# Optimization experiments

Hardware: AMD Instinct MI355X
Metric: run time of the kernel (lower is better)

The kernel has to match this reference:

```python
import jax, jax.numpy as jnp
import numpy as np

B, M, C = 8, 8192, 256   # batch, seeds, seed feature dim
F = 128                  # vote feature dim
P, K = 256, 32           # proposals, samples per group
CA, NCLS = 256, 10       # aggregated feat dim, classes
RADIUS = 0.3


def _lin(x, w, b):
    # 1x1 conv == pointwise linear; w: (out, in)
    return jnp.einsum('...c,oc->...o', x, w) + b


def _bnrelu(x, s, t):
    # eval-mode BatchNorm folded to per-channel affine, then ReLU
    return jnp.maximum(x * s + t, 0.0)


def _fps(xyz, npoint):
    # farthest point sampling; deterministic start at index 0
    Bb, N, _ = xyz.shape
    bidx = jnp.arange(Bb)

    def step(carry, _):
        distance, farthest = carry
        centroid = xyz[bidx, farthest][:, None, :]          # (B,1,2)
        d = jnp.sum((xyz - centroid) ** 2, -1)              # (B,N)
        distance = jnp.minimum(distance, d)
        return (distance, jnp.argmax(distance, -1)), farthest

    init = (jnp.full((Bb, N), 1e10, xyz.dtype), jnp.zeros((Bb,), jnp.int32))
    _, idx = jax.lax.scan(step, init, None, length=npoint)
    return jnp.transpose(idx)                               # (B, npoint)


def _ball_query(xyz, new_xyz, radius, nsample):
    # squared-distance cdist (monotone in euclid dist, so same sort order)
    N = xyz.shape[1]
    d2 = (jnp.sum(new_xyz ** 2, -1)[:, :, None]
          + jnp.sum(xyz ** 2, -1)[:, None, :]
          - 2.0 * jnp.einsum('bsd,bnd->bsn', new_xyz, xyz))  # (B,S,N)
    gidx = jnp.broadcast_to(jnp.arange(N), d2.shape)
    # out-of-radius points replaced by group_first (= index 0, as in source)
    gidx = jnp.where(d2 > radius * radius, 0, gidx)
    order = jnp.argsort(d2, axis=-1)
    return jnp.take_along_axis(gidx, order, axis=-1)[:, :, :nsample]


def _gather(points, idx):
    # points: (B,N,C); idx: (B,...) -> (B,...,C)
    return jax.vmap(lambda p, i: p[i])(points, idx)


def _forward(seed_xyz, seed_feats,
             v_off_w1, v_off_b1, v_off_s1, v_off_t1, v_off_w2, v_off_b2,
             v_ft_w1, v_ft_b1, v_ft_s1, v_ft_t1, v_ft_w2, v_ft_b2,
             a_w1, a_b1, a_s1, a_t1, a_w2, a_b2, a_s2, a_t2,
             p_w1, p_b1, p_s1, p_t1, p_w2, p_b2, p_s2, p_t2,
             obj_w, obj_b, cls_w, cls_b):
    # --- VotingModule (vote_factor=1) ---
    h = _bnrelu(_lin(seed_feats, v_off_w1, v_off_b1), v_off_s1, v_off_t1)
    offsets = _lin(h, v_off_w2, v_off_b2)                   # (B,M,2)
    g = _bnrelu(_lin(seed_feats, v_ft_w1, v_ft_b1), v_ft_s1, v_ft_t1)
    vote_feats = _lin(g, v_ft_w2, v_ft_b2)                  # (B,M,F)
    votes_xyz = seed_xyz + offsets                          # (B,M,2)

    # --- VoteAggregation ---
    fps_idx = _fps(votes_xyz, P)                            # (B,P)
    new_xyz = _gather(votes_xyz, fps_idx)                   # (B,P,2)
    gidx = _ball_query(votes_xyz, new_xyz, RADIUS, K)       # (B,P,K)
    gv = _gather(votes_xyz, gidx)                           # (B,P,K,2)
    gf = _gather(vote_feats, gidx)                          # (B,P,K,F)
    comb = jnp.concatenate([gv - new_xyz[:, :, None, :], gf], -1)  # (B,P,K,F+2)
    x = _bnrelu(_lin(comb, a_w1, a_b1), a_s1, a_t1)
    x = _bnrelu(_lin(x, a_w2, a_b2), a_s2, a_t2)
    pooled = jnp.max(x, axis=2)                             # (B,P,CA)

    # --- ProposalHead ---
    y = _bnrelu(_lin(pooled, p_w1, p_b1), p_s1, p_t1)
    y = _bnrelu(_lin(y, p_w2, p_b2), p_s2, p_t2)
    obj = _lin(y, obj_w, obj_b)[..., 0]                     # (B,P)
    cls = _lin(y, cls_w, cls_b)                             # (B,P,NCLS)
    return (new_xyz, obj, cls)


def setup_inputs() -> dict:
    key = jax.random.key(0)
    keys = iter(jax.random.split(key, 40))

    def w(shape):
        return (jax.random.normal(next(keys), shape) * 0.05).astype(jnp.float32)

    inp = {
        'seed_xyz': jax.random.uniform(next(keys), (B, M, 2), jnp.float32),
        'seed_feats': jax.random.normal(next(keys), (B, M, C), jnp.float32),
        # voting: offset branch
        'v_off_w1': w((C, C)), 'v_off_b1': w((C,)),
        'v_off_s1': 1.0 + w((C,)), 'v_off_t1': w((C,)),
        'v_off_w2': w((2, C)), 'v_off_b2': w((2,)),
        # voting: feature branch
        'v_ft_w1': w((C, C)), 'v_ft_b1': w((C,)),
        'v_ft_s1': 1.0 + w((C,)), 'v_ft_t1': w((C,)),
        'v_ft_w2': w((F, C)), 'v_ft_b2': w((F,)),
        # aggregation MLP
        'a_w1': w((CA, F + 2)), 'a_b1': w((CA,)),
        'a_s1': 1.0 + w((CA,)), 'a_t1': w((CA,)),
        'a_w2': w((CA, CA)), 'a_b2': w((CA,)),
        'a_s2': 1.0 + w((CA,)), 'a_t2': w((CA,)),
        # proposal head
        'p_w1': w((CA, CA)), 'p_b1': w((CA,)),
        'p_s1': 1.0 + w((CA,)), 'p_t1': w((CA,)),
        'p_w2': w((CA // 2, CA)), 'p_b2': w((CA // 2,)),
        'p_s2': 1.0 + w((CA // 2,)), 'p_t2': w((CA // 2,)),
        'obj_w': w((1, CA // 2)), 'obj_b': w((1,)),
        'cls_w': w((NCLS, CA // 2)), 'cls_b': w((NCLS,)),
    }
    return inp


def reference(seed_xyz, seed_feats,
              v_off_w1, v_off_b1, v_off_s1, v_off_t1, v_off_w2, v_off_b2,
              v_ft_w1, v_ft_b1, v_ft_s1, v_ft_t1, v_ft_w2, v_ft_b2,
              a_w1, a_b1, a_s1, a_t1, a_w2, a_b2, a_s2, a_t2,
              p_w1, p_b1, p_s1, p_t1, p_w2, p_b2, p_s2, p_t2,
              obj_w, obj_b, cls_w, cls_b):
    return _forward(seed_xyz, seed_feats,
                    v_off_w1, v_off_b1, v_off_s1, v_off_t1, v_off_w2, v_off_b2,
                    v_ft_w1, v_ft_b1, v_ft_s1, v_ft_t1, v_ft_w2, v_ft_b2,
                    a_w1, a_b1, a_s1, a_t1, a_w2, a_b2, a_s2, a_t2,
                    p_w1, p_b1, p_s1, p_t1, p_w2, p_b2, p_s2, p_t2,
                    obj_w, obj_b, cls_w, cls_b)
```

## Files before the change

### kernel.cpp

```cpp
#include <hip/hip_runtime.h>

typedef __attribute__((ext_vector_type(8))) short bf16x8;
typedef __attribute__((ext_vector_type(4))) float f32x4;
typedef unsigned short u16;
typedef unsigned int u32;
typedef unsigned long long u64;

#define DEV static __device__ __forceinline__
DEV u16 f2bf(float f) { u32 i = __float_as_uint(f); i += 0x7fffu + ((i >> 16) & 1u); return (u16)(i >> 16); }
DEV float bf2f(u16 u) { return __uint_as_float(((u32)u) << 16); }

constexpr int Mn = 8192;
constexpr int Pn = 256;
constexpr int Kn = 32;
constexpr float R2 = 0.09f;

__global__ __launch_bounds__(256, 2) void k_voting_off(
    const float* __restrict__ sxyz,
    const float* __restrict__ sfeat,
    const float* __restrict__ ow1, const float* __restrict__ ob1,
    const float* __restrict__ os1, const float* __restrict__ ot1,
    const float* __restrict__ ow2, const float* __restrict__ ob2,
    float* __restrict__ votes)
{
  __shared__ __align__(16) char vsm[68608];
  float (*Xc)[68]  = (float(*)[68])vsm;
  float (*Wc)[260] = (float(*)[260])(vsm + 4352);
  float (*Hst)[67] = (float(*)[67])vsm;

  const int tid = threadIdx.x;
  const int row0 = blockIdx.x * 64;
  const int wv = tid >> 6, lane = tid & 63;
  const int rr = wv * 16 + (lane >> 5) * 8;
  const int c4 = (lane & 31) * 4;

  float acc[8][8];
#pragma unroll
  for (int r = 0; r < 8; ++r)
#pragma unroll
    for (int j = 0; j < 8; ++j) acc[r][j] = 0.f;

  for (int kc = 0; kc < 16; ++kc) {
    __syncthreads();
    for (int i = tid; i < 256 * 16; i += 256) {
      int o = i >> 4, k = i & 15;
      Wc[k][o] = ow1[o * 256 + kc * 16 + k];
    }
    for (int i = tid; i < 64 * 16; i += 256) {
      int r = i >> 4, k = i & 15;
      Xc[k][r] = sfeat[(row0 + r) * 256 + kc * 16 + k];
    }
    __syncthreads();
#pragma unroll
    for (int k = 0; k < 16; ++k) {
      float4 x0 = *(const float4*)&Xc[k][rr];
      float4 x1 = *(const float4*)&Xc[k][rr + 4];
      float4 w0 = *(const float4*)&Wc[k][c4];
      float4 w1 = *(const float4*)&Wc[k][128 + c4];
      float x[8] = {x0.x, x0.y, x0.z, x0.w, x1.x, x1.y, x1.z, x1.w};
      float w[8] = {w0.x, w0.y, w0.z, w0.w, w1.x, w1.y, w1.z, w1.w};
#pragma unroll
      for (int r = 0; r < 8; ++r)
#pragma unroll
        for (int j = 0; j < 8; ++j)
          acc[r][j] = fmaf(x[r], w[j], acc[r][j]);
    }
  }
  __syncthreads();
#pragma unroll
  for (int j = 0; j < 8; ++j) {
    int o = (j < 4) ? (c4 + j) : (124 + c4 + j);
    float bb = ob1[o], ss = os1[o], tt = ot1[o];
#pragma unroll
    for (int r = 0; r < 8; ++r)
      Hst[o][rr + r] = fmaxf((acc[r][j] + bb) * ss + tt, 0.f);
  }
  __syncthreads();

  if (tid < 128) {
    int r = tid >> 1, o = tid & 1;
    float a = 0.f;
    for (int k = 0; k < 256; ++k)
      a = fmaf(Hst[k][r], ow2[o * 256 + k], a);
    a += ob2[o];
    int row = row0 + r;
    votes[row * 2 + o] = sxyz[row * 2 + o] + a;
  }
}

__global__ __launch_bounds__(512) void k_fps_vf(
    const float* __restrict__ votes, float* __restrict__ nxyz,
    float* __restrict__ out,
    const float* __restrict__ sfeat, const u16* __restrict__ FW1h,
    const float* __restrict__ fb1, const float* __restrict__ fs1,
    const float* __restrict__ ft1, const u16* __restrict__ FW2b,
    const float* __restrict__ fb2, u16* __restrict__ vfeat)
{
  __shared__ __align__(16) char smem[86016];
  const int tid = threadIdx.x;

  if (blockIdx.x < 8) {
    const int b = blockIdx.x;
    const float* vb = votes + b * Mn * 2;
    float2* xy   = (float2*)smem;
    u32*   Sd    = (u32*)(smem + 65536);
    u32*   Sl    = (u32*)(smem + 65536 + 256);
    float* histx = (float*)(smem + 66048);
    float* histy = (float*)(smem + 67072);

    {
      const float4* vb4 = (const float4*)vb;
#pragma unroll
      for (int j = tid; j < Mn / 2; j += 512) {
        float4 v = vb4[j];
        *(float4*)&xy[2 * j] = v;
      }
    }
    float dist[16];
#pragma unroll
    for (int s = 0; s < 16; ++s) dist[s] = 1e10f;
    __syncthreads();

    float cx = xy[0].x, cy = xy[0].y;
    if (tid == 0) { histx[0] = cx; histy[0] = cy; }

    for (int it = 1; it < Pn; ++it) {
      float bd = -1.f; int sb = 0;
#pragma unroll
      for (int s = 0; s < 16; ++s) {
        float2 p = xy[s * 512 + tid];
        float dx = p.x - cx, dy = p.y - cy;
        float d = fminf(dist[s], dx * dx + dy * dy);
        dist[s] = d;
        if (d > bd) { bd = d; sb = s; }
      }
      int bi = sb * 512 + tid;

      u32 hd = __float_as_uint(bd), hl = ~(u32)bi;

#define FPS_ROR(VD, VL, N)                                                      \
      {                                                                         \
        u32 od = (u32)__builtin_amdgcn_update_dpp(0, (int)VD, 0x120 + N, 0xF, 0xF, false); \
        u32 ol = (u32)__builtin_amdgcn_update_dpp(0, (int)VL, 0x120 + N, 0xF, 0xF, false); \
        bool g = (od > VD) || (od == VD && ol > VL);                            \
        VD = g ? od : VD; VL = g ? ol : VL;                                     \
      }
      FPS_ROR(hd, hl, 8)
      FPS_ROR(hd, hl, 4)
      FPS_ROR(hd, hl, 2)
      FPS_ROR(hd, hl, 1)

      const int buf = it & 1;
      if ((tid & 15) == 0) {
        int row = tid >> 4;
        Sd[buf * 32 + row] = hd; Sl[buf * 32 + row] = hl;
      }
      __syncthreads();

      int rr = tid & 15;
      u32 rd = Sd[buf * 32 + rr], rl = Sl[buf * 32 + rr];
      {
        u32 od = Sd[buf * 32 + 16 + rr], ol = Sl[buf * 32 + 16 + rr];
        bool g = (od > rd) || (od == rd && ol > rl);
        rd = g ? od : rd; rl = g ? ol : rl;
      }
      FPS_ROR(rd, rl, 8)
      FPS_ROR(rd, rl, 4)
      FPS_ROR(rd, rl, 2)
      FPS_ROR(rd, rl, 1)
#undef FPS_ROR

      int widx = (int)(~rl);
      float2 w = xy[widx];
      cx = w.x; cy = w.y;
      if (tid == 0) { histx[it] = cx; histy[it] = cy; }
    }
    __syncthreads();
    if (tid < 256) {
      float2 o2; o2.x = histx[tid]; o2.y = histy[tid];
      *(float2*)&nxyz[(b * Pn + tid) * 2] = o2;
      *(float2*)&out[(b * Pn + tid) * 2] = o2;
    }
  } else {
    const int bx = blockIdx.x - 8;
    const int row0 = bx * 128;
    u16* Hs = (u16*)smem;
    u16* As = (u16*)(smem + 34816);
    u16* Bs = (u16*)(smem + 45056);

    const int wid = tid >> 6, lane = tid & 63, m16 = lane & 15, quad = lane >> 4;
    const int wr = wid >> 2;
    const int wc4 = wid & 3;
    const int sr = tid >> 2, sk = (tid & 3) * 8;

    f32x4 acc2[4][2];
#pragma unroll
    for (int mt = 0; mt < 4; ++mt)
#pragma unroll
      for (int nt = 0; nt < 2; ++nt) acc2[mt][nt] = (f32x4){0.f, 0.f, 0.f, 0.f};

    for (int h = 0; h < 2; ++h) {
      f32x4 acc[4][2];
#pragma unroll
      for (int mt = 0; mt < 4; ++mt)
#pragma unroll
        for (int nt = 0; nt < 2; ++nt) acc[mt][nt] = (f32x4){0.f, 0.f, 0.f, 0.f};

      for (int s = 0; s < 8; ++s) {
        __syncthreads();
        {
          const float* src = &sfeat[(row0 + sr) * 256 + s * 32 + sk];
          float4 v0 = *(const float4*)&src[0];
          float4 v1 = *(const float4*)&src[4];
          u32 packed[4];
          packed[0] = (u32)f2bf(v0.x) | ((u32)f2bf(v0.y) << 16);
          packed[1] = (u32)f2bf(v0.z) | ((u32)f2bf(v0.w) << 16);
          packed[2] = (u32)f2bf(v1.x) | ((u32)f2bf(v1.y) << 16);
          packed[3] = (u32)f2bf(v1.z) | ((u32)f2bf(v1.w) << 16);
          *(uint4*)&As[sr * 40 + sk] = *(uint4*)&packed[0];
          *(uint4*)&Bs[sr * 40 + sk] =
              *(const uint4*)&FW1h[(h * 128 + sr) * 256 + s * 32 + sk];
        }
        __syncthreads();
#pragma unroll
        for (int mt = 0; mt < 4; ++mt) {
          bf16x8 af = *(const bf16x8*)&As[(wr * 64 + mt * 16 + m16) * 40 + quad * 8];
#pragma unroll
          for (int nt = 0; nt < 2; ++nt) {
            bf16x8 bfr = *(const bf16x8*)&Bs[(wc4 * 32 + nt * 16 + m16) * 40 + quad * 8];
            acc[mt][nt] = __builtin_amdgcn_mfma_f32_16x16x32_bf16(af, bfr, acc[mt][nt], 0, 0, 0);
          }
        }
      }
      __syncthreads();
#pragma unroll
      for (int nt = 0; nt < 2; ++nt) {
        int colL = wc4 * 32 + nt * 16 + m16;
        int col = h * 128 + colL;
        float bb = fb1[col], ss = fs1[col], tt = ft1[col];
#pragma unroll
        for (int mt = 0; mt < 4; ++mt) {
          int rL = wr * 64 + mt * 16 + quad * 4;
#pragma unroll
          for (int r = 0; r < 4; ++r)
            Hs[(rL + r) * 136 + colL] = f2bf(fmaxf((acc[mt][nt][r] + bb) * ss + tt, 0.f));
        }
      }
      for (int s2 = 0; s2 < 4; ++s2) {
        __syncthreads();
        {
          *(uint4*)&Bs[sr * 40 + sk] =
              *(const uint4*)&FW2b[sr * 256 + h * 128 + s2 * 32 + sk];
        }
        __syncthreads();
#pragma unroll
        for (int mt = 0; mt < 4; ++mt) {
          bf16x8 af = *(const bf16x8*)&Hs[(wr * 64 + mt * 16 + m16) * 136 + s2 * 32 + quad * 8];
#pragma unroll
          for (int nt = 0; nt < 2; ++nt) {
            bf16x8 bfr = *(const bf16x8*)&Bs[(wc4 * 32 + nt * 16 + m16) * 40 + quad * 8];
            acc2[mt][nt] = __builtin_amdgcn_mfma_f32_16x16x32_bf16(af, bfr, acc2[mt][nt], 0, 0, 0);
          }
        }
      }
    }
#pragma unroll
    for (int nt = 0; nt < 2; ++nt) {
      int col = wc4 * 32 + nt * 16 + m16;
      float bb = fb2[col];
#pragma unroll
      for (int mt = 0; mt < 4; ++mt) {
        int rbase = row0 + wr * 64 + mt * 16 + quad * 4;
#pragma unroll
        for (int r = 0; r < 4; ++r)
          vfeat[(rbase + r) * 128 + col] = f2bf(acc2[mt][nt][r] + bb);
      }
    }
  }
}

__global__ __launch_bounds__(256) void k_ballq(
    const float* __restrict__ votes, const float* __restrict__ nxyz,
    int* __restrict__ gidx)
{
  const int bp = blockIdx.x, tid = threadIdx.x;
  const int b = bp >> 8;
  const float* vb = votes + b * Mn * 2;
  const float sx = nxyz[bp * 2], sy = nxyz[bp * 2 + 1];
  const float a = sx * sx + sy * sy;
  float d2[32];
#pragma unroll
  for (int s = 0; s < 32; ++s) {
    int i = tid * 32 + s;
    float x = vb[i * 2], y = vb[i * 2 + 1];
    d2[s] = (a + (x * x + y * y)) - 2.f * (sx * x + sy * y);
  }
  __shared__ float sd[4];
  __shared__ int si[4];
  __shared__ int swi;
  unsigned mask = 0;
  for (int kk = 0; kk < Kn; ++kk) {
    float bd = 3.4e38f; int bi = 0x7fffffff;
#pragma unroll
    for (int s = 0; s < 32; ++s)
      if (!((mask >> s) & 1u) && d2[s] < bd) { bd = d2[s]; bi = tid * 32 + s; }
#pragma unroll
    for (int off = 32; off > 0; off >>= 1) {
      float od = __shfl_xor(bd, off);
      int oi = __shfl_xor(bi, off);
      if (od < bd || (od == bd && oi < bi)) { bd = od; bi = oi; }
    }
    if ((tid & 63) == 0) { sd[tid >> 6] = bd; si[tid >> 6] = bi; }
    __syncthreads();
    if (tid == 0) {
#pragma unroll
      for (int w = 1; w < 4; ++w)
        if (sd[w] < bd || (sd[w] == bd && si[w] < bi)) { bd = sd[w]; bi = si[w]; }
      swi = bi;
      gidx[bp * Kn + kk] = (bd > R2) ? 0 : bi;
    }
    __syncthreads();
    int wi = swi;
    if ((wi >> 5) == tid) mask |= 1u << (wi & 31);
  }
}

__global__ __launch_bounds__(256) void k_prep(
    const float* __restrict__ fw1, const float* __restrict__ fw2,
    const float* __restrict__ aw1, const float* __restrict__ aw2,
    u16* __restrict__ FW1h, u16* __restrict__ FW2b,
    u16* __restrict__ AW1b, u16* __restrict__ AW2b)
{
  const int gid = blockIdx.x * 256 + threadIdx.x;
  const int gsz = gridDim.x * 256;
  for (int i = gid; i < 65536; i += gsz) FW1h[i] = f2bf(fw1[i]);
  for (int i = gid; i < 32768; i += gsz) FW2b[i] = f2bf(fw2[i]);
  for (int i = gid; i < 65536; i += gsz) AW2b[i] = f2bf(aw2[i]);
  for (int i = gid; i < 49152; i += gsz) {
    int o = i / 192, k = i % 192;
    AW1b[i] = (k < 130) ? f2bf(aw1[o * 130 + k]) : (u16)0;
  }
}

__global__ __launch_bounds__(256) void k_agg_head(
    const float* __restrict__ votes, const u16* __restrict__ vfeat,
    const float* __restrict__ nxyz, const int* __restrict__ gidx,
    const u16* __restrict__ AW1b, const float* __restrict__ ab1,
    const float* __restrict__ as1, const float* __restrict__ at1,
    const u16* __restrict__ AW2b, const float* __restrict__ ab2,
    const float* __restrict__ as2, const float* __restrict__ at2,
    const float* __restrict__ pw1, const float* __restrict__ pb1,
    const float* __restrict__ ps1, const float* __restrict__ pt1,
    const float* __restrict__ pw2, const float* __restrict__ pb2,
    const float* __restrict__ ps2, const float* __restrict__ pt2,
    const float* __restrict__ objw, const float* __restrict__ objb,
    const float* __restrict__ clsw, const float* __restrict__ clsb,
    float* __restrict__ out)
{
  __shared__ u16 U[32 * 264];
  __shared__ u16 Bs[256 * 72];
  __shared__ int gix[32];
  __shared__ float gvx[32], gvy[32];
  u16* CombA = U;
  u16* As = U;
  float* x2T = (float*)Bs;
  float* xr = (float*)U;
  float* y1 = ((float*)U) + 256;
  float* y2 = ((float*)U) + 512;

  const int bp = blockIdx.x, tid = threadIdx.x, b = bp >> 8;
  if (tid < 32) {
    int g = gidx[bp * 32 + tid];
    gix[tid] = g;
    gvx[tid] = votes[(b * Mn + g) * 2];
    gvy[tid] = votes[(b * Mn + g) * 2 + 1];
  }
  __syncthreads();
  const float sx = nxyz[bp * 2], sy = nxyz[bp * 2 + 1];

  if (tid < 192) {
    int row = tid / 6, c = tid % 6;
    const u16* vsrc = &vfeat[(b * Mn + gix[row]) * 128];
    u16* dst = &CombA[row * 200 + c * 32];
    if (c == 0) {
      dst[0] = f2bf(gvx[row] - sx);
      dst[1] = f2bf(gvy[row] - sy);
      for (int k = 2; k < 32; ++k) dst[k] = vsrc[k - 2];
    } else if (c <= 3) {
      for (int k = 0; k < 32; ++k) dst[k] = vsrc[c * 32 + k - 2];
    } else if (c == 4) {
      dst[0] = vsrc[126]; dst[1] = vsrc[127];
      for (int k = 2; k < 32; ++k) dst[k] = 0;
    } else {
      for (int k = 0; k < 32; ++k) dst[k] = 0;
    }
  }

  const int wid = tid >> 6, lane = tid & 63, m16 = lane & 15, quad = lane >> 4;
  const int mt = wid & 1, nh = wid >> 1;

  f32x4 acc[8];
#pragma unroll
  for (int nt = 0; nt < 8; ++nt) acc[nt] = (f32x4){0.f, 0.f, 0.f, 0.f};
  for (int s = 0; s < 3; ++s) {
    __syncthreads();
    for (int i = tid; i < 4096; i += 256) {
      int n = i >> 4, c4 = i & 15;
      *(uint2*)&Bs[n * 72 + c4 * 4] = *(const uint2*)&AW1b[n * 192 + s * 64 + c4 * 4];
    }
    __syncthreads();
#pragma unroll
    for (int ks = 0; ks < 2; ++ks) {
      bf16x8 af = *(const bf16x8*)&CombA[(mt * 16 + m16) * 200 + s * 64 + ks * 32 + quad * 8];
#pragma unroll
      for (int nt = 0; nt < 8; ++nt) {
        bf16x8 bf_ = *(const bf16x8*)&Bs[(nh * 128 + nt * 16 + m16) * 72 + ks * 32 + quad * 8];
        acc[nt] = __builtin_amdgcn_mfma_f32_16x16x32_bf16(af, bf_, acc[nt], 0, 0, 0);
      }
    }
  }
  __syncthreads();
#pragma unroll
  for (int nt = 0; nt < 8; ++nt) {
    int col = nh * 128 + nt * 16 + m16;
    float bb = ab1[col], ss = as1[col], tt = at1[col];
#pragma unroll
    for (int r = 0; r < 4; ++r) {
      int samp = mt * 16 + quad * 4 + r;
      As[samp * 264 + col] = f2bf(fmaxf((acc[nt][r] + bb) * ss + tt, 0.f));
    }
  }

  f32x4 acc2[8];
#pragma unroll
  for (int nt = 0; nt < 8; ++nt) acc2[nt] = (f32x4){0.f, 0.f, 0.f, 0.f};
  for (int s = 0; s < 4; ++s) {
    __syncthreads();
    for (int i = tid; i < 4096; i += 256) {
      int n = i >> 4, c4 = i & 15;
      *(uint2*)&Bs[n * 72 + c4 * 4] = *(const uint2*)&AW2b[n * 256 + s * 64 + c4 * 4];
    }
    __syncthreads();
#pragma unroll
    for (int ks = 0; ks < 2; ++ks) {
      bf16x8 af = *(const bf16x8*)&As[(mt * 16 + m16) * 264 + s * 64 + ks * 32 + quad * 8];
#pragma unroll
      for (int nt = 0; nt < 8; ++nt) {
        bf16x8 bf_ = *(const bf16x8*)&Bs[(nh * 128 + nt * 16 + m16) * 72 + ks * 32 + quad * 8];
        acc2[nt] = __builtin_amdgcn_mfma_f32_16x16x32_bf16(af, bf_, acc2[nt], 0, 0, 0);
      }
    }
  }
  __syncthreads();
#pragma unroll
  for (int nt = 0; nt < 8; ++nt) {
    int col = nh * 128 + nt * 16 + m16;
    float bb = ab2[col], ss = as2[col], tt = at2[col];
#pragma unroll
    for (int r = 0; r < 4; ++r) {
      int samp = mt * 16 + quad * 4 + r;
      x2T[col * 33 + samp] = fmaxf((acc2[nt][r] + bb) * ss + tt, 0.f);
    }
  }
  __syncthreads();
  {
    float m = x2T[tid * 33];
#pragma unroll
    for (int s2 = 1; s2 < 32; ++s2) m = fmaxf(m, x2T[tid * 33 + s2]);
    xr[tid] = m;
  }
  __syncthreads();

  {
    float a = 0.f;
    for (int c = 0; c < 256; ++c) a = fmaf(xr[c], pw1[tid * 256 + c], a);
    a = (a + pb1[tid]) * ps1[tid] + pt1[tid];
    y1[tid] = fmaxf(a, 0.f);
  }
  __syncthreads();
  if (tid < 128) {
    float a = 0.f;
    for (int c = 0; c < 256; ++c) a = fmaf(y1[c], pw2[tid * 256 + c], a);
    a = (a + pb2[tid]) * ps2[tid] + pt2[tid];
    y2[tid] = fmaxf(a, 0.f);
  }
  __syncthreads();
  if (tid < 10) {
    float a = 0.f;
    for (int c = 0; c < 128; ++c) a = fmaf(y2[c], clsw[tid * 128 + c], a);
    out[6144 + bp * 10 + tid] = a + clsb[tid];
  } else if (tid == 10) {
    float a = 0.f;
    for (int c = 0; c < 128; ++c) a = fmaf(y2[c], objw[c], a);
    out[4096 + bp] = a + objb[0];
  }
}

extern "C" void kernel_launch(void* const* d_in, const int* in_sizes, int n_in,
                              void* d_out, int out_size, void* d_ws, size_t ws_size,
                              hipStream_t stream)
{
  (void)in_sizes; (void)n_in; (void)out_size; (void)ws_size;
  const float* sxyz  = (const float*)d_in[0];
  const float* sfeat = (const float*)d_in[1];
  const float* ow1 = (const float*)d_in[2];
  const float* ob1 = (const float*)d_in[3];
  const float* os1 = (const float*)d_in[4];
  const float* ot1 = (const float*)d_in[5];
  const float* ow2 = (const float*)d_in[6];
  const float* ob2 = (const float*)d_in[7];
  const float* fw1 = (const float*)d_in[8];
  const float* fb1 = (const float*)d_in[9];
  const float* fs1 = (const float*)d_in[10];
  const float* ft1 = (const float*)d_in[11];
  const float* fw2 = (const float*)d_in[12];
  const float* fb2 = (const float*)d_in[13];
  const float* aw1 = (const float*)d_in[14];
  const float* ab1 = (const float*)d_in[15];
  const float* as1 = (const float*)d_in[16];
  const float* at1 = (const float*)d_in[17];
  const float* aw2 = (const float*)d_in[18];
  const float* ab2 = (const float*)d_in[19];
  const float* as2 = (const float*)d_in[20];
  const float* at2 = (const float*)d_in[21];
  const float* pw1 = (const float*)d_in[22];
  const float* pb1 = (const float*)d_in[23];
  const float* ps1 = (const float*)d_in[24];
  const float* pt1 = (const float*)d_in[25];
  const float* pw2 = (const float*)d_in[26];
  const float* pb2 = (const float*)d_in[27];
  const float* ps2 = (const float*)d_in[28];
  const float* pt2 = (const float*)d_in[29];
  const float* objw = (const float*)d_in[30];
  const float* objb = (const float*)d_in[31];
  const float* clsw = (const float*)d_in[32];
  const float* clsb = (const float*)d_in[33];

  char* ws = (char*)d_ws;
  float* votes  = (float*)(ws + 0);
  u16*   vfeat  = (u16*)  (ws + 524288);
  float* nxyz   = (float*)(ws + 17301504);
  int*   gidxp  = (int*)  (ws + 17317888);
  u16*   FW1h   = (u16*)  (ws + 19677184);
  u16*   FW2b   = (u16*)  (ws + 19808256);
  u16*   AW1b   = (u16*)  (ws + 19873792);
  u16*   AW2b   = (u16*)  (ws + 19972096);
  float* out    = (float*)d_out;

  k_prep<<<dim3(256), dim3(256), 0, stream>>>(
      fw1, fw2, aw1, aw2, FW1h, FW2b, AW1b, AW2b);

  k_voting_off<<<dim3(1024), dim3(256), 0, stream>>>(
      sxyz, sfeat, ow1, ob1, os1, ot1, ow2, ob2, votes);

  k_fps_vf<<<dim3(520), dim3(512), 0, stream>>>(
      votes, nxyz, out,
      sfeat, FW1h, fb1, fs1, ft1, FW2b, fb2, vfeat);

  k_ballq<<<dim3(2048), dim3(256), 0, stream>>>(votes, nxyz, gidxp);

  k_agg_head<<<dim3(2048), dim3(256), 0, stream>>>(
      votes, vfeat, nxyz, gidxp, AW1b, ab1, as1, at1,
      AW2b, ab2, as2, at2,
      pw1, pb1, ps1, pt1, pw2, pb2, ps2, pt2,
      objw, objb, clsw, clsb, out);
}
```

Measured before the change: 854.9 us.

## Fuse ball query into aggregation head and vectorize FPS LDS loads

The standalone ball-query kernel is merged into the aggregation/head kernel. Each block now computes its 32 neighbour indices directly into shared memory, which removes one kernel launch and the global round-trip of the index array. Separately, the FPS inner loop reads two points per float4 LDS load, which changes the point-to-thread mapping from strided to paired and halves the number of shared-memory load instructions per iteration. The fused kernel carries the d2[32] register array, which may raise register pressure in the head kernel.

```diff
diff --git a/kernel.cpp b/kernel.cpp
--- a/kernel.cpp
+++ b/kernel.cpp
@@ -125,16 +125,20 @@
     if (tid == 0) { histx[0] = cx; histy[0] = cy; }
 
     for (int it = 1; it < Pn; ++it) {
-      float bd = -1.f; int sb = 0;
-#pragma unroll
-      for (int s = 0; s < 16; ++s) {
-        float2 p = xy[s * 512 + tid];
-        float dx = p.x - cx, dy = p.y - cy;
-        float d = fminf(dist[s], dx * dx + dy * dy);
-        dist[s] = d;
-        if (d > bd) { bd = d; sb = s; }
-      }
-      int bi = sb * 512 + tid;
+      float bd = -1.f; int bi = 0;
+#pragma unroll
+      for (int s = 0; s < 8; ++s) {
+        int base = s * 1024 + 2 * tid;
+        float4 p2 = *(const float4*)&xy[base];
+        float dx0 = p2.x - cx, dy0 = p2.y - cy;
+        float d0 = fminf(dist[2 * s], dx0 * dx0 + dy0 * dy0);
+        dist[2 * s] = d0;
+        if (d0 > bd) { bd = d0; bi = base; }
+        float dx1 = p2.z - cx, dy1 = p2.w - cy;
+        float d1 = fminf(dist[2 * s + 1], dx1 * dx1 + dy1 * dy1);
+        dist[2 * s + 1] = d1;
+        if (d1 > bd) { bd = d1; bi = base + 1; }
+      }
 
       u32 hd = __float_as_uint(bd), hl = ~(u32)bi;
 
@@ -279,52 +283,6 @@
   }
 }
 
-__global__ __launch_bounds__(256) void k_ballq(
-    const float* __restrict__ votes, const float* __restrict__ nxyz,
-    int* __restrict__ gidx)
-{
-  const int bp = blockIdx.x, tid = threadIdx.x;
-  const int b = bp >> 8;
-  const float* vb = votes + b * Mn * 2;
-  const float sx = nxyz[bp * 2], sy = nxyz[bp * 2 + 1];
-  const float a = sx * sx + sy * sy;
-  float d2[32];
-#pragma unroll
-  for (int s = 0; s < 32; ++s) {
-    int i = tid * 32 + s;
-    float x = vb[i * 2], y = vb[i * 2 + 1];
-    d2[s] = (a + (x * x + y * y)) - 2.f * (sx * x + sy * y);
-  }
-  __shared__ float sd[4];
-  __shared__ int si[4];
-  __shared__ int swi;
-  unsigned mask = 0;
-  for (int kk = 0; kk < Kn; ++kk) {
-    float bd = 3.4e38f; int bi = 0x7fffffff;
-#pragma unroll
-    for (int s = 0; s < 32; ++s)
-      if (!((mask >> s) & 1u) && d2[s] < bd) { bd = d2[s]; bi = tid * 32 + s; }
-#pragma unroll
-    for (int off = 32; off > 0; off >>= 1) {
-      float od = __shfl_xor(bd, off);
-      int oi = __shfl_xor(bi, off);
-      if (od < bd || (od == bd && oi < bi)) { bd = od; bi = oi; }
-    }
-    if ((tid & 63) == 0) { sd[tid >> 6] = bd; si[tid >> 6] = bi; }
-    __syncthreads();
-    if (tid == 0) {
-#pragma unroll
-      for (int w = 1; w < 4; ++w)
-        if (sd[w] < bd || (sd[w] == bd && si[w] < bi)) { bd = sd[w]; bi = si[w]; }
-      swi = bi;
-      gidx[bp * Kn + kk] = (bd > R2) ? 0 : bi;
-    }
-    __syncthreads();
-    int wi = swi;
-    if ((wi >> 5) == tid) mask |= 1u << (wi & 31);
-  }
-}
-
 __global__ __launch_bounds__(256) void k_prep(
     const float* __restrict__ fw1, const float* __restrict__ fw2,
     const float* __restrict__ aw1, const float* __restrict__ aw2,
@@ -342,9 +300,9 @@
   }
 }
 
-__global__ __launch_bounds__(256) void k_agg_head(
+__global__ __launch_bounds__(256) void k_ballq_agg_head(
     const float* __restrict__ votes, const u16* __restrict__ vfeat,
-    const float* __restrict__ nxyz, const int* __restrict__ gidx,
+    const float* __restrict__ nxyz,
     const u16* __restrict__ AW1b, const float* __restrict__ ab1,
     const float* __restrict__ as1, const float* __restrict__ at1,
     const u16* __restrict__ AW2b, const float* __restrict__ ab2,
@@ -361,6 +319,9 @@
   __shared__ u16 Bs[256 * 72];
   __shared__ int gix[32];
   __shared__ float gvx[32], gvy[32];
+  __shared__ float sd[4];
+  __shared__ int si[4];
+  __shared__ int swi;
   u16* CombA = U;
   u16* As = U;
   float* x2T = (float*)Bs;
@@ -369,9 +330,48 @@
   float* y2 = ((float*)U) + 512;
 
   const int bp = blockIdx.x, tid = threadIdx.x, b = bp >> 8;
+
+  {
+    const float* vb = votes + b * Mn * 2;
+    const float sx0 = nxyz[bp * 2], sy0 = nxyz[bp * 2 + 1];
+    const float a = sx0 * sx0 + sy0 * sy0;
+    float d2[32];
+#pragma unroll
+    for (int s = 0; s < 32; ++s) {
+      int i = tid * 32 + s;
+      float x = vb[i * 2], y = vb[i * 2 + 1];
+      d2[s] = (a + (x * x + y * y)) - 2.f * (sx0 * x + sy0 * y);
+    }
+    unsigned mask = 0;
+    for (int kk = 0; kk < Kn; ++kk) {
+      float bd = 3.4e38f; int bi = 0x7fffffff;
+#pragma unroll
+      for (int s = 0; s < 32; ++s)
+        if (!((mask >> s) & 1u) && d2[s] < bd) { bd = d2[s]; bi = tid * 32 + s; }
+#pragma unroll
+      for (int off = 32; off > 0; off >>= 1) {
+        float od = __shfl_xor(bd, off);
+        int oi = __shfl_xor(bi, off);
+        if (od < bd || (od == bd && oi < bi)) { bd = od; bi = oi; }
+      }
+      if ((tid & 63) == 0) { sd[tid >> 6] = bd; si[tid >> 6] = bi; }
+      __syncthreads();
+      if (tid == 0) {
+#pragma unroll
+        for (int w = 1; w < 4; ++w)
+          if (sd[w] < bd || (sd[w] == bd && si[w] < bi)) { bd = sd[w]; bi = si[w]; }
+        swi = bi;
+        gix[kk] = (bd > R2) ? 0 : bi;
+      }
+      __syncthreads();
+      int wi = swi;
+      if ((wi >> 5) == tid) mask |= 1u << (wi & 31);
+    }
+  }
+  __syncthreads();
+
   if (tid < 32) {
-    int g = gidx[bp * 32 + tid];
-    gix[tid] = g;
+    int g = gix[tid];
     gvx[tid] = votes[(b * Mn + g) * 2];
     gvy[tid] = votes[(b * Mn + g) * 2 + 1];
   }
@@ -540,7 +540,6 @@
   float* votes  = (float*)(ws + 0);
   u16*   vfeat  = (u16*)  (ws + 524288);
   float* nxyz   = (float*)(ws + 17301504);
-  int*   gidxp  = (int*)  (ws + 17317888);
   u16*   FW1h   = (u16*)  (ws + 19677184);
   u16*   FW2b   = (u16*)  (ws + 19808256);
   u16*   AW1b   = (u16*)  (ws + 19873792);
@@ -557,10 +556,8 @@
       votes, nxyz, out,
       sfeat, FW1h, fb1, fs1, ft1, FW2b, fb2, vfeat);
 
-  k_ballq<<<dim3(2048), dim3(256), 0, stream>>>(votes, nxyz, gidxp);
-
-  k_agg_head<<<dim3(2048), dim3(256), 0, stream>>>(
-      votes, vfeat, nxyz, gidxp, AW1b, ab1, as1, at1,
+  k_ballq_agg_head<<<dim3(2048), dim3(256), 0, stream>>>(
+      votes, vfeat, nxyz, AW1b, ab1, as1, at1,
       AW2b, ab2, as2, at2,
       pw1, pb1, ps1, pt1, pw2, pb2, ps2, pt2,
       objw, objb, clsw, clsb, out);
```

Result: slower. 927.5 us (+8.5%).
